# Kernel tuning notes

Hardware: AMD Instinct MI355X
Metric: run time of the kernel (lower is better)

## Reference

```python
import jax, jax.numpy as jnp
import numpy as np

N, M, D = 32768, 4096, 128  # samples, SOM units (64x64), input_dim
GRID_H, GRID_W = 64, 64


def setup_inputs() -> dict:
    key = jax.random.key(0)
    k1, k2 = jax.random.split(key)
    inputs = jax.random.normal(k1, (N, D), dtype=jnp.float32)
    # SOM2D.__init__: weights = torch.rand(size, input_dim)
    weights = jax.random.uniform(k2, (M, D), dtype=jnp.float32)
    # grid = meshgrid(arange(H), arange(W)) -> [M, 2] integer unit coordinates
    gx, gy = jnp.meshgrid(jnp.arange(GRID_H), jnp.arange(GRID_W), indexing='ij')
    grid = jnp.stack([gx, gy], axis=-1).reshape(-1, 2).astype(jnp.int32)
    return {"inputs": inputs, "weights": weights, "grid": grid}


def reference(inputs, weights, grid):
    # sed(x, y): squared Euclidean distance [N, M].
    # tensor the torch code materializes; same math.
    x_sq = jnp.sum(inputs * inputs, axis=1, keepdims=True)        # [N, 1]
    w_sq = jnp.sum(weights * weights, axis=1)                      # [M]
    cross = jnp.einsum('nd,md->nm', inputs, weights)               # [N, M]
    distances = x_sq + w_sq - 2.0 * cross                          # [N, M]
    # wtac: argmin over units, then lookup grid coordinates of the winner.
    winning_indices = jnp.argmin(distances, axis=1)                # [N]
    winning_labels = grid[winning_indices]                         # [N, 2]
    return winning_labels
```

## Files before the change

kernel.cpp:

```cpp
#include <hip/hip_runtime.h>
#include <float.h>
#include <stdint.h>


constexpr int D = 128;

typedef _Float16 f16x8 __attribute__((ext_vector_type(8)));
typedef float    f32x4 __attribute__((ext_vector_type(4)));

__device__ __forceinline__ void cvt_split(const float4& a0, const float4& a1,
                                          f16x8& h, f16x8& l) {
    float v[8] = {a0.x, a0.y, a0.z, a0.w, a1.x, a1.y, a1.z, a1.w};
#pragma unroll
    for (int j = 0; j < 8; ++j) {
        _Float16 hh = (_Float16)v[j];
        h[j] = hh;
        l[j] = (_Float16)(v[j] - (float)hh);
    }
}

__global__ __launch_bounds__(256) void prep_kernel(
        const float* __restrict__ w, f16x8* __restrict__ hG,
        f16x8* __restrict__ lG, float* __restrict__ wsq, int M) {
    int g = blockIdx.x * 256 + threadIdx.x;
    if (g >= M * 16) return;
    int u = g >> 4, o = g & 15;
    const float4* wp = reinterpret_cast<const float4*>(w + (size_t)u * D + o * 8);
    float4 a0 = wp[0], a1 = wp[1];
    f16x8 h, l;
    cvt_split(a0, a1, h, l);
    float ss = 0.f;
    ss = fmaf(a0.x, a0.x, ss); ss = fmaf(a0.y, a0.y, ss);
    ss = fmaf(a0.z, a0.z, ss); ss = fmaf(a0.w, a0.w, ss);
    ss = fmaf(a1.x, a1.x, ss); ss = fmaf(a1.y, a1.y, ss);
    ss = fmaf(a1.z, a1.z, ss); ss = fmaf(a1.w, a1.w, ss);
#pragma unroll
    for (int m = 1; m < 16; m <<= 1) ss += __shfl_xor(ss, m, 64);
    if (o == 0) wsq[u] = ss;
    int slot = ((u >> 5) << 9) + ((o >> 2) << 7) + (((u >> 4) & 1) << 6)
             + ((o & 3) << 4) + (u & 15);
    hG[slot] = h;
    lG[slot] = l;
}

__global__ void finalize(const unsigned long long* __restrict__ keys,
                         const int* __restrict__ grid, int* __restrict__ out,
                         int N, int UG) {
    int s = blockIdx.x * blockDim.x + threadIdx.x;
    if (s >= N) return;
    unsigned long long k = keys[s];
    for (int g = 1; g < UG; ++g) {
        unsigned long long kg = keys[(size_t)g * N + s];
        if (kg < k) k = kg;
    }
    int idx = (int)(unsigned)(k & 0xFFFFFFFFull);
    out[2 * s]     = grid[2 * idx];
    out[2 * s + 1] = grid[2 * idx + 1];
}

template <bool PARTIAL>
__global__ __launch_bounds__(256, 2) void som_main(
        const float* __restrict__ x, const f16x8* __restrict__ hG,
        const f16x8* __restrict__ lG, const float* __restrict__ wsq,
        const int* __restrict__ grid, int* __restrict__ out,
        unsigned long long* __restrict__ keys,
        int unitGroups, int M, int N) {
    __shared__ f16x8 albuf[4 * 1024];

    const int tid  = threadIdx.x;
    const int lane = tid & 63;
    const int wv   = tid >> 6;
    const int c    = lane & 15;
    const int q    = lane >> 4;

    const int ug    = blockIdx.x % unitGroups;
    const int sg    = blockIdx.x / unitGroups;
    const int sWave = sg * 256 + wv * 64;

    f16x8* myAl = &albuf[wv * 1024];

    f16x8 Ah[16];
#pragma unroll
    for (int i = 0; i < 4; ++i) {
        const float* xr = x + (size_t)(sWave + 16 * i + c) * D + q * 8;
#pragma unroll
        for (int s = 0; s < 4; ++s) {
            float4 a0 = *reinterpret_cast<const float4*>(xr + 32 * s);
            float4 a1 = *reinterpret_cast<const float4*>(xr + 32 * s + 4);
            f16x8 h, l;
            cvt_split(a0, a1, h, l);
            Ah[i * 4 + s] = h;
            myAl[(i * 4 + s) * 64 + lane] = l;
        }
    }

    float bestD[16];
    int   bestI[16];
#pragma unroll
    for (int sl = 0; sl < 16; ++sl) { bestD[sl] = FLT_MAX; bestI[sl] = 0; }

    const int tilesPer = (M / 32) / unitGroups;
    const int tile0    = ug * tilesPer;

    for (int tt = 0; tt < tilesPer; ++tt) {
        const int tile = tile0 + tt;
        const f16x8* hp = hG + ((size_t)tile << 9) + lane;
        const f16x8* lp = lG + ((size_t)tile << 9) + lane;

        f16x8 bh[8], bl[8];
#pragma unroll
        for (int s = 0; s < 4; ++s)
#pragma unroll
            for (int t = 0; t < 2; ++t)
                bh[s * 2 + t] = hp[s * 128 + t * 64];
#pragma unroll
        for (int s = 0; s < 4; ++s)
#pragma unroll
            for (int t = 0; t < 2; ++t)
                bl[s * 2 + t] = lp[s * 128 + t * 64];

        const int uTile = tile * 32;
        const float wq0 = wsq[uTile + c];
        const float wq1 = wsq[uTile + 16 + c];

        f32x4 acc[8];
#pragma unroll
        for (int f = 0; f < 8; ++f) acc[f] = (f32x4){0.f, 0.f, 0.f, 0.f};

#pragma unroll
        for (int s = 0; s < 4; ++s)
#pragma unroll
            for (int i = 0; i < 4; ++i)
#pragma unroll
                for (int t = 0; t < 2; ++t)
                    acc[i * 2 + t] = __builtin_amdgcn_mfma_f32_16x16x32_f16(
                        Ah[i * 4 + s], bh[s * 2 + t], acc[i * 2 + t], 0, 0, 0);
#pragma unroll
        for (int s = 0; s < 4; ++s) {
            f16x8 al[4];
#pragma unroll
            for (int i = 0; i < 4; ++i) al[i] = myAl[(i * 4 + s) * 64 + lane];
#pragma unroll
            for (int i = 0; i < 4; ++i)
#pragma unroll
                for (int t = 0; t < 2; ++t)
                    acc[i * 2 + t] = __builtin_amdgcn_mfma_f32_16x16x32_f16(
                        al[i], bh[s * 2 + t], acc[i * 2 + t], 0, 0, 0);
        }
#pragma unroll
        for (int s = 0; s < 4; ++s)
#pragma unroll
            for (int i = 0; i < 4; ++i)
#pragma unroll
                for (int t = 0; t < 2; ++t)
                    acc[i * 2 + t] = __builtin_amdgcn_mfma_f32_16x16x32_f16(
                        Ah[i * 4 + s], bl[s * 2 + t], acc[i * 2 + t], 0, 0, 0);

#pragma unroll
        for (int t = 0; t < 2; ++t) {
            const int n    = uTile + 16 * t + c;
            const float wq = t == 0 ? wq0 : wq1;
#pragma unroll
            for (int i = 0; i < 4; ++i) {
                f32x4 a = acc[i * 2 + t];
#pragma unroll
                for (int r = 0; r < 4; ++r) {
                    float score = fmaf(-2.f, a[r], wq);
                    int sl = i * 4 + r;
                    if (score < bestD[sl]) { bestD[sl] = score; bestI[sl] = n; }
                }
            }
        }
    }

#pragma unroll
    for (int sl = 0; sl < 16; ++sl) {
        float d   = bestD[sl];
        int   idx = bestI[sl];
#pragma unroll
        for (int m = 1; m < 16; m <<= 1) {
            float od = __shfl_xor(d, m, 64);
            int   oi = __shfl_xor(idx, m, 64);
            if (od < d || (od == d && oi < idx)) { d = od; idx = oi; }
        }
        if (c == 0) {
            const int sOut = sWave + 16 * (sl >> 2) + 4 * q + (sl & 3);
            if (PARTIAL) {
                unsigned ub = __float_as_uint(d);
                ub = (ub & 0x80000000u) ? ~ub : (ub | 0x80000000u);
                unsigned long long key = ((unsigned long long)ub << 32) | (unsigned)idx;
                keys[(size_t)ug * N + sOut] = key;
            } else {
                out[2 * sOut]     = grid[2 * idx];
                out[2 * sOut + 1] = grid[2 * idx + 1];
            }
        }
    }
}

extern "C" void kernel_launch(void* const* d_in, const int* in_sizes, int n_in,
                              void* d_out, int out_size, void* d_ws, size_t ws_size,
                              hipStream_t stream) {
    const float* x    = (const float*)d_in[0];
    const float* w    = (const float*)d_in[1];
    const int*   grid = (const int*)d_in[2];
    int* out = (int*)d_out;

    const int N = in_sizes[0] / D;
    const int M = in_sizes[1] / D;

    const size_t hlBytes   = (size_t)M * D * 2;
    const size_t baseBytes = 2 * hlBytes + (size_t)M * 4;

    f16x8* hG  = (f16x8*)d_ws;
    f16x8* lG  = (f16x8*)((char*)d_ws + hlBytes);
    float* wsq = (float*)((char*)d_ws + 2 * hlBytes);
    unsigned long long* keys = (unsigned long long*)((char*)d_ws + baseBytes);

    prep_kernel<<<(M * 16 + 255) / 256, 256, 0, stream>>>(w, hG, lG, wsq, M);

    const int sampleGroups = N / 256;
    int UG = 0;
    if (ws_size >= baseBytes + 4ull * N * 8) UG = 4;
    else if (ws_size >= baseBytes + 2ull * N * 8) UG = 2;

    if (UG > 0) {
        som_main<true><<<sampleGroups * UG, 256, 0, stream>>>(
            x, hG, lG, wsq, grid, out, keys, UG, M, N);
        finalize<<<(N + 255) / 256, 256, 0, stream>>>(keys, grid, out, N, UG);
    } else {
        som_main<false><<<sampleGroups, 256, 0, stream>>>(
            x, hG, lG, wsq, grid, out, nullptr, 1, M, N);
    }
}
```

Before: 154.9 us.

## Prefetch next weight tile in registers and fuse finalize via last-block atomic counter

The weight hi/lo fragments for the next tile are now loaded into registers while the current tile's MFMAs run, instead of being loaded at the top of each iteration. The separate finalize kernel is removed: each block bumps a per-sample-group atomic counter, and the last block to finish reduces the partial keys and writes the grid labels. This is meant to hide global load latency and drop one kernel launch, at the cost of more live registers (possible spills with launch bounds 2) and extra fences and atomics. The counters are zeroed inside prep_kernel.

```diff
diff --git a/kernel.cpp b/kernel.cpp
--- a/kernel.cpp
+++ b/kernel.cpp
@@ -21,7 +21,9 @@
 
 __global__ __launch_bounds__(256) void prep_kernel(
         const float* __restrict__ w, f16x8* __restrict__ hG,
-        f16x8* __restrict__ lG, float* __restrict__ wsq, int M) {
+        f16x8* __restrict__ lG, float* __restrict__ wsq,
+        int* __restrict__ cnt, int nGroups, int M) {
+    if (cnt && blockIdx.x == 0 && (int)threadIdx.x < nGroups) cnt[threadIdx.x] = 0;
     int g = blockIdx.x * 256 + threadIdx.x;
     if (g >= M * 16) return;
     int u = g >> 4, o = g & 15;
@@ -43,29 +45,15 @@
     lG[slot] = l;
 }
 
-__global__ void finalize(const unsigned long long* __restrict__ keys,
-                         const int* __restrict__ grid, int* __restrict__ out,
-                         int N, int UG) {
-    int s = blockIdx.x * blockDim.x + threadIdx.x;
-    if (s >= N) return;
-    unsigned long long k = keys[s];
-    for (int g = 1; g < UG; ++g) {
-        unsigned long long kg = keys[(size_t)g * N + s];
-        if (kg < k) k = kg;
-    }
-    int idx = (int)(unsigned)(k & 0xFFFFFFFFull);
-    out[2 * s]     = grid[2 * idx];
-    out[2 * s + 1] = grid[2 * idx + 1];
-}
-
 template <bool PARTIAL>
 __global__ __launch_bounds__(256, 2) void som_main(
         const float* __restrict__ x, const f16x8* __restrict__ hG,
         const f16x8* __restrict__ lG, const float* __restrict__ wsq,
         const int* __restrict__ grid, int* __restrict__ out,
-        unsigned long long* __restrict__ keys,
+        unsigned long long* __restrict__ keys, int* __restrict__ cnt,
         int unitGroups, int M, int N) {
     __shared__ f16x8 albuf[4 * 1024];
+    __shared__ int lastFlag;
 
     const int tid  = threadIdx.x;
     const int lane = tid & 63;
@@ -102,22 +90,24 @@
     const int tilesPer = (M / 32) / unitGroups;
     const int tile0    = ug * tilesPer;
 
+    f16x8 bh[8], bl[8];
+    {
+        const f16x8* hp = hG + ((size_t)tile0 << 9) + lane;
+        const f16x8* lp = lG + ((size_t)tile0 << 9) + lane;
+#pragma unroll
+        for (int s = 0; s < 4; ++s)
+#pragma unroll
+            for (int t = 0; t < 2; ++t) {
+                bh[s * 2 + t] = hp[s * 128 + t * 64];
+                bl[s * 2 + t] = lp[s * 128 + t * 64];
+            }
+    }
+
     for (int tt = 0; tt < tilesPer; ++tt) {
-        const int tile = tile0 + tt;
-        const f16x8* hp = hG + ((size_t)tile << 9) + lane;
-        const f16x8* lp = lG + ((size_t)tile << 9) + lane;
-
-        f16x8 bh[8], bl[8];
-#pragma unroll
-        for (int s = 0; s < 4; ++s)
-#pragma unroll
-            for (int t = 0; t < 2; ++t)
-                bh[s * 2 + t] = hp[s * 128 + t * 64];
-#pragma unroll
-        for (int s = 0; s < 4; ++s)
-#pragma unroll
-            for (int t = 0; t < 2; ++t)
-                bl[s * 2 + t] = lp[s * 128 + t * 64];
+        const int tile  = tile0 + tt;
+        const int tileN = (tt + 1 < tilesPer) ? tile + 1 : tile;
+        const f16x8* hpn = hG + ((size_t)tileN << 9) + lane;
+        const f16x8* lpn = lG + ((size_t)tileN << 9) + lane;
 
         const int uTile = tile * 32;
         const float wq0 = wsq[uTile + c];
@@ -150,11 +140,22 @@
 #pragma unroll
         for (int s = 0; s < 4; ++s)
 #pragma unroll
+            for (int t = 0; t < 2; ++t)
+                bh[s * 2 + t] = hpn[s * 128 + t * 64];
+
+#pragma unroll
+        for (int s = 0; s < 4; ++s)
+#pragma unroll
             for (int i = 0; i < 4; ++i)
 #pragma unroll
                 for (int t = 0; t < 2; ++t)
                     acc[i * 2 + t] = __builtin_amdgcn_mfma_f32_16x16x32_f16(
                         Ah[i * 4 + s], bl[s * 2 + t], acc[i * 2 + t], 0, 0, 0);
+#pragma unroll
+        for (int s = 0; s < 4; ++s)
+#pragma unroll
+            for (int t = 0; t < 2; ++t)
+                bl[s * 2 + t] = lpn[s * 128 + t * 64];
 
 #pragma unroll
         for (int t = 0; t < 2; ++t) {
@@ -196,6 +197,28 @@
             }
         }
     }
+
+    if (PARTIAL) {
+        __threadfence();
+        __syncthreads();
+        if (tid == 0) {
+            int old = atomicAdd(&cnt[sg], 1);
+            lastFlag = (old == unitGroups - 1);
+        }
+        __syncthreads();
+        if (lastFlag) {
+            __threadfence();
+            const int s = sg * 256 + tid;
+            unsigned long long k = keys[s];
+            for (int g = 1; g < unitGroups; ++g) {
+                unsigned long long kg = keys[(size_t)g * N + s];
+                if (kg < k) k = kg;
+            }
+            const int idx = (int)(unsigned)(k & 0xFFFFFFFFull);
+            out[2 * s]     = grid[2 * idx];
+            out[2 * s + 1] = grid[2 * idx + 1];
+        }
+    }
 }
 
 extern "C" void kernel_launch(void* const* d_in, const int* in_sizes, int n_in,
@@ -208,6 +231,7 @@
 
     const int N = in_sizes[0] / D;
     const int M = in_sizes[1] / D;
+    const int nGroups = N / 256;
 
     const size_t hlBytes   = (size_t)M * D * 2;
     const size_t baseBytes = 2 * hlBytes + (size_t)M * 4;
@@ -215,21 +239,22 @@
     f16x8* hG  = (f16x8*)d_ws;
     f16x8* lG  = (f16x8*)((char*)d_ws + hlBytes);
     float* wsq = (float*)((char*)d_ws + 2 * hlBytes);
+
+    int UG = 0;
+    if (ws_size >= baseBytes + 4ull * N * 8 + (size_t)nGroups * 4) UG = 4;
+    else if (ws_size >= baseBytes + 2ull * N * 8 + (size_t)nGroups * 4) UG = 2;
+
     unsigned long long* keys = (unsigned long long*)((char*)d_ws + baseBytes);
-
-    prep_kernel<<<(M * 16 + 255) / 256, 256, 0, stream>>>(w, hG, lG, wsq, M);
-
-    const int sampleGroups = N / 256;
-    int UG = 0;
-    if (ws_size >= baseBytes + 4ull * N * 8) UG = 4;
-    else if (ws_size >= baseBytes + 2ull * N * 8) UG = 2;
+    int* cnt = (int*)((char*)d_ws + baseBytes + (size_t)UG * N * 8);
+
+    prep_kernel<<<(M * 16 + 255) / 256, 256, 0, stream>>>(
+        w, hG, lG, wsq, UG > 0 ? cnt : nullptr, nGroups, M);
 
     if (UG > 0) {
-        som_main<true><<<sampleGroups * UG, 256, 0, stream>>>(
-            x, hG, lG, wsq, grid, out, keys, UG, M, N);
-        finalize<<<(N + 255) / 256, 256, 0, stream>>>(keys, grid, out, N, UG);
+        som_main<true><<<nGroups * UG, 256, 0, stream>>>(
+            x, hG, lG, wsq, grid, out, keys, cnt, UG, M, N);
     } else {
-        som_main<false><<<sampleGroups, 256, 0, stream>>>(
-            x, hG, lG, wsq, grid, out, nullptr, 1, M, N);
-    }
-}
+        som_main<false><<<nGroups, 256, 0, stream>>>(
+            x, hG, lG, wsq, grid, out, nullptr, nullptr, 1, M, N);
+    }
+}
```

After: 215.5 us. +39.1%, slower.
